# Kernel tuning notes

Hardware: AMD Instinct MI355X
Metric: run time of the kernel (lower is better)

The kernel has to match this reference:

```python
import jax, jax.numpy as jnp
import numpy as np

MULTI_INFER_NUM = 8
D_EMBED = 128
T, B = 256, 32


def setup_inputs() -> dict:
    key = jax.random.key(0)
    k1, k2, k3, k4 = jax.random.split(key, 4)
    positions = jax.random.randint(k1, (T, B), 0, 12, dtype=jnp.int64)
    outputs = jax.random.normal(k2, (T, B, D_EMBED), dtype=jnp.float32)
    W = jax.random.normal(k3, (MULTI_INFER_NUM + 1, D_EMBED, D_EMBED), dtype=jnp.float32)
    b = jax.random.normal(k4, (MULTI_INFER_NUM + 1, D_EMBED), dtype=jnp.float32)
    return {"positions": positions, "outputs": outputs, "W": W, "b": b}


def reference(positions, outputs, W, b):
    # Clamp positions >= multi_infer_num to the last (overflow) expert slot.
    r_pos = jnp.where(positions < MULTI_INFER_NUM, positions, MULTI_INFER_NUM)  # [T,B]
    # Gather per-token d x d transfer matrix, then batched matvec + bias,
    # matching tf.nn.embedding_lookup + einsum('ibde,ibd->ibe').
    w_gathered = W[r_pos]                         # [T,B,d,d]
    y = jnp.einsum('tbde,tbd->tbe', w_gathered, outputs)
    y = y + b[r_pos]                              # [T,B,d]
    return y
```

## Files before the change

kernel.cpp:

```cpp
#include <hip/hip_runtime.h>
#include <cstdint>

#define D 128
#define NEXP 9
#define TPB 256
#define CH0 512
#define CH8 128

__device__ __forceinline__ uint32_t pack2_bf16(float a, float b) {
    uint32_t ua = __builtin_bit_cast(uint32_t, a);
    uint32_t ub = __builtin_bit_cast(uint32_t, b);
    ua += 0x7fffu + ((ua >> 16) & 1u);
    ub += 0x7fffu + ((ub >> 16) & 1u);
    return (ua >> 16) | (ub & 0xffff0000u);
}

__global__ __launch_bounds__(TPB) void ltf_kernel(
    const int* __restrict__ pos, const float* __restrict__ x,
    const float* __restrict__ W, const float* __restrict__ bias,
    float* __restrict__ y, int ntok, int c0)
{
    __shared__ uint32_t Wp[D * (D / 2)];
    __shared__ float XT[4][D * 8];
    __shared__ int lst[CH0];
    __shared__ int cnt;

    const int tid = threadIdx.x;
    const int lane = tid & 63;
    const int wv = tid >> 6;
    const int bid = blockIdx.x;

    int r, start, C;
    if (bid < 8 * c0) { r = bid / c0; start = (bid - r * c0) * CH0; C = CH0; }
    else              { r = 8; start = (bid - 8 * c0) * CH8; C = CH8; }

    if (tid == 0) cnt = 0;
    __syncthreads();

    const int end = (start + C < ntok) ? start + C : ntok;
    #pragma unroll
    for (int it = 0; it < CH0 / TPB; ++it) {
        int t = start + it * TPB + tid;
        bool m = false;
        if (t < end) {
            int p = pos[t];
            int rp = p < (NEXP - 1) ? p : (NEXP - 1);
            m = (rp == r);
        }
        unsigned long long mask = __ballot(m);
        int nm = __popcll(mask);
        int base = 0;
        if (lane == 0 && nm > 0) base = atomicAdd(&cnt, nm);
        base = __shfl(base, 0);
        if (m) {
            int pre = __popcll(mask & ((1ull << lane) - 1ull));
            lst[base + pre] = t;
        }
    }

    const float4* Wr4 = reinterpret_cast<const float4*>(W + (size_t)r * D * D);
    #pragma unroll
    for (int i = 0; i < (D * D / 4) / TPB; ++i) {
        int idx = i * TPB + tid;
        float4 w = Wr4[idx];
        Wp[idx * 2 + 0] = pack2_bf16(w.x, w.y);
        Wp[idx * 2 + 1] = pack2_bf16(w.z, w.w);
    }
    __syncthreads();

    const int nc = cnt;
    float* xt = XT[wv];
    const float2 bv = reinterpret_cast<const float2*>(bias + (size_t)r * D)[lane];

    for (int g = wv; g * 8 < nc; g += 4) {
        const int gb = g * 8;
        int valid = nc - gb; if (valid > 8) valid = 8;

        const int ti = lane >> 3, seg = lane & 7;
        int tsel = ti < valid ? ti : valid - 1;
        int mytok = lst[gb + tsel];
        const float4* xs = reinterpret_cast<const float4*>(x + (size_t)mytok * D + seg * 16);
        #pragma unroll
        for (int j = 0; j < 4; ++j) {
            float4 v = xs[j];
            int d0 = seg * 16 + j * 4;
            xt[(d0 + 0) * 8 + ti] = v.x;
            xt[(d0 + 1) * 8 + ti] = v.y;
            xt[(d0 + 2) * 8 + ti] = v.z;
            xt[(d0 + 3) * 8 + ti] = v.w;
        }

        float a0[8], a1[8];
        #pragma unroll
        for (int t = 0; t < 8; ++t) { a0[t] = 0.f; a1[t] = 0.f; }

        #pragma unroll 4
        for (int d = 0; d < D; ++d) {
            uint32_t w2 = Wp[d * 64 + lane];
            float w0 = __builtin_bit_cast(float, w2 << 16);
            float w1 = __builtin_bit_cast(float, w2 & 0xffff0000u);
            const float4* xr = reinterpret_cast<const float4*>(&xt[d * 8]);
            float4 va = xr[0];
            float4 vb = xr[1];
            a0[0] += w0 * va.x; a1[0] += w1 * va.x;
            a0[1] += w0 * va.y; a1[1] += w1 * va.y;
            a0[2] += w0 * va.z; a1[2] += w1 * va.z;
            a0[3] += w0 * va.w; a1[3] += w1 * va.w;
            a0[4] += w0 * vb.x; a1[4] += w1 * vb.x;
            a0[5] += w0 * vb.y; a1[5] += w1 * vb.y;
            a0[6] += w0 * vb.z; a1[6] += w1 * vb.z;
            a0[7] += w0 * vb.w; a1[7] += w1 * vb.w;
        }

        #pragma unroll
        for (int t = 0; t < 8; ++t) {
            if (t < valid) {
                int tk = lst[gb + t];
                float2 o;
                o.x = a0[t] + bv.x;
                o.y = a1[t] + bv.y;
                reinterpret_cast<float2*>(y + (size_t)tk * D)[lane] = o;
            }
        }
    }
}

extern "C" void kernel_launch(void* const* d_in, const int* in_sizes, int n_in,
                              void* d_out, int out_size, void* d_ws, size_t ws_size,
                              hipStream_t stream) {
    const int* pos  = (const int*)d_in[0];
    const float* x  = (const float*)d_in[1];
    const float* W  = (const float*)d_in[2];
    const float* b  = (const float*)d_in[3];
    float* y = (float*)d_out;

    const int ntok = in_sizes[0];
    const int c0 = (ntok + CH0 - 1) / CH0;
    const int c8 = (ntok + CH8 - 1) / CH8;
    ltf_kernel<<<8 * c0 + c8, TPB, 0, stream>>>(pos, x, W, b, y, ntok, c0);
}
```

Baseline: 76.72 us.

## Replace scalar FMA matvec loop with bf16 MFMA 16x16x32 tiles

Recasts the per-expert token matvecs as a small GEMM on matrix cores. The expert weight matrix is repacked into shared memory in bf16 MFMA B-fragment layout. Each wave takes 16 tokens and builds bf16 A fragments directly from global x, so the transposed-x shared buffer goes away. The intent is to replace the VALU-bound FMA loop with MFMA instructions. In exchange, activations are now rounded to bf16 as well, output stores are scattered 4-byte writes instead of float2, and the weight staging does strided scalar global reads.

```diff
diff --git a/kernel.cpp b/kernel.cpp
--- a/kernel.cpp
+++ b/kernel.cpp
@@ -6,6 +6,11 @@
 #define TPB 256
 #define CH0 512
 #define CH8 128
+
+typedef __bf16 bf16x8_t __attribute__((ext_vector_type(8)));
+typedef float  f32x4_t  __attribute__((ext_vector_type(4)));
+
+union FragA { uint32_t u[4]; bf16x8_t v; };
 
 __device__ __forceinline__ uint32_t pack2_bf16(float a, float b) {
     uint32_t ua = __builtin_bit_cast(uint32_t, a);
@@ -20,15 +25,14 @@
     const float* __restrict__ W, const float* __restrict__ bias,
     float* __restrict__ y, int ntok, int c0)
 {
-    __shared__ uint32_t Wp[D * (D / 2)];
-    __shared__ float XT[4][D * 8];
+    __shared__ uint32_t Wf[8192];
     __shared__ int lst[CH0];
     __shared__ int cnt;
 
-    const int tid = threadIdx.x;
+    const int tid  = threadIdx.x;
     const int lane = tid & 63;
-    const int wv = tid >> 6;
-    const int bid = blockIdx.x;
+    const int wv   = tid >> 6;
+    const int bid  = blockIdx.x;
 
     int r, start, C;
     if (bid < 8 * c0) { r = bid / c0; start = (bid - r * c0) * CH0; C = CH0; }
@@ -58,68 +62,69 @@
         }
     }
 
-    const float4* Wr4 = reinterpret_cast<const float4*>(W + (size_t)r * D * D);
+    const float* Wr = W + (size_t)r * D * D;
     #pragma unroll
-    for (int i = 0; i < (D * D / 4) / TPB; ++i) {
-        int idx = i * TPB + tid;
-        float4 w = Wr4[idx];
-        Wp[idx * 2 + 0] = pack2_bf16(w.x, w.y);
-        Wp[idx * 2 + 1] = pack2_bf16(w.z, w.w);
+    for (int i = 0; i < 8; ++i) {
+        int s = i * TPB + tid;
+        int l = s & 63, T = s >> 6;
+        int q = l >> 4, m = l & 15;
+        int kt = T >> 3, n = T & 7;
+        const float* src = Wr + (kt * 32 + q * 8) * D + n * 16 + m;
+        uint32_t u0 = pack2_bf16(src[0 * D], src[1 * D]);
+        uint32_t u1 = pack2_bf16(src[2 * D], src[3 * D]);
+        uint32_t u2 = pack2_bf16(src[4 * D], src[5 * D]);
+        uint32_t u3 = pack2_bf16(src[6 * D], src[7 * D]);
+        *reinterpret_cast<uint4*>(&Wf[s * 4]) = uint4{u0, u1, u2, u3};
     }
     __syncthreads();
 
     const int nc = cnt;
-    float* xt = XT[wv];
-    const float2 bv = reinterpret_cast<const float2*>(bias + (size_t)r * D)[lane];
+    const int q = lane >> 4, mloc = lane & 15;
 
-    for (int g = wv; g * 8 < nc; g += 4) {
-        const int gb = g * 8;
-        int valid = nc - gb; if (valid > 8) valid = 8;
+    float bvn[8];
+    #pragma unroll
+    for (int n = 0; n < 8; ++n) bvn[n] = bias[(size_t)r * D + n * 16 + mloc];
 
-        const int ti = lane >> 3, seg = lane & 7;
-        int tsel = ti < valid ? ti : valid - 1;
-        int mytok = lst[gb + tsel];
-        const float4* xs = reinterpret_cast<const float4*>(x + (size_t)mytok * D + seg * 16);
+    const int rounds = (nc + 63) >> 6;
+    for (int rd = 0; rd < rounds; ++rd) {
+        const int b16 = rd * 64 + wv * 16;
+        if (b16 >= nc) continue;
+
+        int ta = b16 + mloc; if (ta >= nc) ta = nc - 1;
+        const int tokA = lst[ta];
+        const float4* xrow = reinterpret_cast<const float4*>(x + (size_t)tokA * D);
+
+        f32x4_t acc[8];
         #pragma unroll
-        for (int j = 0; j < 4; ++j) {
-            float4 v = xs[j];
-            int d0 = seg * 16 + j * 4;
-            xt[(d0 + 0) * 8 + ti] = v.x;
-            xt[(d0 + 1) * 8 + ti] = v.y;
-            xt[(d0 + 2) * 8 + ti] = v.z;
-            xt[(d0 + 3) * 8 + ti] = v.w;
-        }
+        for (int n = 0; n < 8; ++n) acc[n] = f32x4_t{0.f, 0.f, 0.f, 0.f};
 
-        float a0[8], a1[8];
         #pragma unroll
-        for (int t = 0; t < 8; ++t) { a0[t] = 0.f; a1[t] = 0.f; }
-
-        #pragma unroll 4
-        for (int d = 0; d < D; ++d) {
-            uint32_t w2 = Wp[d * 64 + lane];
-            float w0 = __builtin_bit_cast(float, w2 << 16);
-            float w1 = __builtin_bit_cast(float, w2 & 0xffff0000u);
-            const float4* xr = reinterpret_cast<const float4*>(&xt[d * 8]);
-            float4 va = xr[0];
-            float4 vb = xr[1];
-            a0[0] += w0 * va.x; a1[0] += w1 * va.x;
-            a0[1] += w0 * va.y; a1[1] += w1 * va.y;
-            a0[2] += w0 * va.z; a1[2] += w1 * va.z;
-            a0[3] += w0 * va.w; a1[3] += w1 * va.w;
-            a0[4] += w0 * vb.x; a1[4] += w1 * vb.x;
-            a0[5] += w0 * vb.y; a1[5] += w1 * vb.y;
-            a0[6] += w0 * vb.z; a1[6] += w1 * vb.z;
-            a0[7] += w0 * vb.w; a1[7] += w1 * vb.w;
+        for (int kt = 0; kt < 4; ++kt) {
+            float4 va = xrow[kt * 8 + q * 2];
+            float4 vb = xrow[kt * 8 + q * 2 + 1];
+            FragA a;
+            a.u[0] = pack2_bf16(va.x, va.y);
+            a.u[1] = pack2_bf16(va.z, va.w);
+            a.u[2] = pack2_bf16(vb.x, vb.y);
+            a.u[3] = pack2_bf16(vb.z, vb.w);
+            #pragma unroll
+            for (int n = 0; n < 8; ++n) {
+                bf16x8_t bf = *reinterpret_cast<const bf16x8_t*>(
+                    &Wf[(kt * 8 + n) * 256 + lane * 4]);
+                acc[n] = __builtin_amdgcn_mfma_f32_16x16x32_bf16(
+                    a.v, bf, acc[n], 0, 0, 0);
+            }
         }
 
         #pragma unroll
-        for (int t = 0; t < 8; ++t) {
-            if (t < valid) {
-                int tk = lst[gb + t];
-                float2 o;
-                o.x = a0[t] + bv.x;
-                o.y = a1[t] + bv.y;
-                reinterpret_cast<float2*>(y + (size_t)tk * D)[lane] = o;
+        for (int reg = 0; reg < 4; ++reg) {
+            int tloc = b16 + q * 4 + reg;
+            if (tloc < nc) {
+                int tok = lst[tloc];
+                float* yr = y + (size_t)tok * D + mloc;
+                #pragma unroll
+                for (int n = 0; n < 8; ++n)
+                    yr[n * 16] = acc[n][reg] + bvn[n];
             }
         }
     }
```

Measured after the change: 66.46 us. 13.4% less time.
